# Optimization experiments

Hardware: AMD Instinct MI355X
Metric: run time of the kernel (lower is better)

Reference implementation:

```python
import jax, jax.numpy as jnp
import numpy as np

VAR_N, LEVELS, NCELLS, PRED_N = 4, 17, 56, 12
D = VAR_N * LEVELS          # 68
FLAT = VAR_N * D            # 272 = ntiles * interm in CrossConnector
T = 4096
DT = 0.1                    # fused-ODE solver step of the LTC cell


def _var_encoder(x, w1, b1, w2, b2, w3, b3, w4, b4, w5, b5):
    # nn.Sequential(Linear, ReLU, Linear, ReLU, Linear, ReLU, Linear, ReLU, Linear)
    h = jax.nn.relu(x @ w1 + b1)
    h = jax.nn.relu(h @ w2 + b2)
    h = jax.nn.relu(h @ w3 + b3)
    h = jax.nn.relu(h @ w4 + b4)
    return h @ w5 + b5


def _run_ltc(seq, wx, wh, b, a, tau, wout, bout):
    def cell(h, u):
        f = jax.nn.sigmoid(u @ wx + h @ wh + b)           # gated synaptic activation
        return (h + DT * f * a) / (1.0 + DT * (1.0 / (tau + 0.5) + f))

    def step_obs(h, u):
        h2 = cell(h, u)
        return h2, h2 @ wout + bout

    hT, vs1 = jax.lax.scan(step_obs, jnp.zeros((NCELLS,), seq.dtype), seq)

    def step_pred(carry, _):
        h, v = carry
        h2 = cell(h, v)
        v2 = h2 @ wout + bout
        return (h2, v2), v2

    _, vs2 = jax.lax.scan(step_pred, (hT, vs1[-1]), None, length=PRED_N)
    return jnp.concatenate([vs1, vs2], axis=0)        # (T+PRED_N, LEVELS)


def setup_inputs() -> dict:
    key = jax.random.key(0)
    ks = iter(jax.random.split(key, 64))
    d = {"x": jax.random.normal(next(ks), (T, D), jnp.float32)}

    def add_ve(prefix, inp, out):
        dims = [(inp, inp), (inp, inp), (inp, out), (out, out), (out, out)]
        for i, (fi, fo) in enumerate(dims, 1):
            d[f"{prefix}w{i}"] = jax.random.normal(next(ks), (fi, fo), jnp.float32) / np.sqrt(fi)
            d[f"{prefix}b{i}"] = jax.random.normal(next(ks), (fo,), jnp.float32) * 0.01

    add_ve("p", D, D)          # preproc  VarEncoder(68,68)
    add_ve("c1", LEVELS, D)    # CrossConnector inner VarEncoder(17,68)
    add_ve("c2", FLAT, D)      # CrossConnector outer VarEncoder(272,68)

    d["ltc_wx"] = jax.random.normal(next(ks), (VAR_N, LEVELS, NCELLS), jnp.float32) / np.sqrt(LEVELS)
    d["ltc_wh"] = jax.random.normal(next(ks), (VAR_N, NCELLS, NCELLS), jnp.float32) / np.sqrt(NCELLS)
    d["ltc_b"] = jax.random.normal(next(ks), (VAR_N, NCELLS), jnp.float32) * 0.01
    d["ltc_a"] = jax.random.normal(next(ks), (VAR_N, NCELLS), jnp.float32)
    d["ltc_tau"] = jax.random.uniform(next(ks), (VAR_N, NCELLS), jnp.float32)
    d["ltc_wout"] = jax.random.normal(next(ks), (VAR_N, NCELLS, LEVELS), jnp.float32) / np.sqrt(NCELLS)
    d["ltc_bout"] = jax.random.normal(next(ks), (VAR_N, LEVELS), jnp.float32) * 0.01
    return d


def reference(x, pw1, pb1, pw2, pb2, pw3, pb3, pw4, pb4, pw5, pb5,
              c1w1, c1b1, c1w2, c1b2, c1w3, c1b3, c1w4, c1b4, c1w5, c1b5,
              c2w1, c2b1, c2w2, c2b2, c2w3, c2b3, c2w4, c2b4, c2w5, c2b5,
              ltc_wx, ltc_wh, ltc_b, ltc_a, ltc_tau, ltc_wout, ltc_bout):
    pre = _var_encoder(x, pw1, pb1, pw2, pb2, pw3, pb3, pw4, pb4, pw5, pb5)   # (T, 68)
    xs = pre.reshape(VAR_N, -1, LEVELS)                                       # (4, T, 17) row-major, as torch.reshape
    vs = jax.vmap(_run_ltc)(xs, ltc_wx, ltc_wh, ltc_b, ltc_a, ltc_tau,
                            ltc_wout, ltc_bout)                               # (4, T+12, 17)
    vs = jnp.transpose(vs, (1, 0, 2))                                         # (T+12, 4, 17)
    y = jax.nn.relu(_var_encoder(vs, c1w1, c1b1, c1w2, c1b2, c1w3, c1b3,
                                 c1w4, c1b4, c1w5, c1b5))                     # (T+12, 4, 68)
    y = y.reshape(y.shape[0], -1)                                             # (T+12, 272)
    return _var_encoder(y, c2w1, c2b1, c2w2, c2b2, c2w3, c2b3,
                        c2w4, c2b4, c2w5, c2b5)                               # (T+12, 68)
```

## Files before the change

### kernel.cpp

```cpp
#include <hip/hip_runtime.h>
#include <hip/hip_bf16.h>
#include <math.h>

#define VAR_N 4
#define LEVELS 17
#define NCELLS 56
#define PRED_N 12
#define TSTEPS 4096
#define DT 0.1f
#define RPB 8
#define LOG2E 1.44269504088896340736f

static __device__ __forceinline__ float rl(float x, int lane) {
    return __int_as_float(__builtin_amdgcn_readlane(__float_as_int(x), lane));
}
static __device__ __forceinline__ float rcpf(float x) {
    return __builtin_amdgcn_rcpf(x);
}

template <int S>
__global__ void mlp5_kernel(const float* __restrict__ in, float* __restrict__ out,
                            const float* __restrict__ w1, const float* __restrict__ b1,
                            const float* __restrict__ w2, const float* __restrict__ b2,
                            const float* __restrict__ w3, const float* __restrict__ b3,
                            const float* __restrict__ w4, const float* __restrict__ b4,
                            const float* __restrict__ w5, const float* __restrict__ b5,
                            int nrows, int d0, int d1, int d2, int d3, int d4, int d5,
                            int relu_last) {
    extern __shared__ float lds[];
    float* bufA = lds;
    float* bufB = lds + RPB * S;
    const int r0 = blockIdx.x * RPB;
    const int tid = threadIdx.x;
    const int bt = blockDim.x;

    for (int idx = tid; idx < RPB * d0; idx += bt) {
        int r = idx / d0, c = idx - r * d0;
        int gr = r0 + r;
        bufA[r * S + c] = (gr < nrows) ? in[(size_t)gr * d0 + c] : 0.f;
    }
    __syncthreads();

    const float* Ws[5] = {w1, w2, w3, w4, w5};
    const float* Bs[5] = {b1, b2, b3, b4, b5};
    int dins[5] = {d0, d1, d2, d3, d4};
    int douts[5] = {d1, d2, d3, d4, d5};

    for (int L = 0; L < 5; ++L) {
        const float* __restrict__ W = Ws[L];
        const float* __restrict__ B = Bs[L];
        const int din = dins[L], dout = douts[L];
        const bool act = (L < 4) || (relu_last != 0);
        for (int j = tid; j < dout; j += bt) {
            float acc[RPB];
            float bj = B[j];
#pragma unroll
            for (int r = 0; r < RPB; ++r) acc[r] = bj;
            int k = 0;
            for (; k + 4 <= din; k += 4) {
                float w0v = W[(size_t)(k + 0) * dout + j];
                float w1v = W[(size_t)(k + 1) * dout + j];
                float w2v = W[(size_t)(k + 2) * dout + j];
                float w3v = W[(size_t)(k + 3) * dout + j];
#pragma unroll
                for (int r = 0; r < RPB; ++r) {
                    const float4 hx = *(const float4*)(bufA + r * S + k);
                    acc[r] = fmaf(hx.x, w0v,
                              fmaf(hx.y, w1v,
                               fmaf(hx.z, w2v,
                                fmaf(hx.w, w3v, acc[r]))));
                }
            }
            for (; k < din; ++k) {
                float wv = W[(size_t)k * dout + j];
#pragma unroll
                for (int r = 0; r < RPB; ++r)
                    acc[r] = fmaf(bufA[r * S + k], wv, acc[r]);
            }
#pragma unroll
            for (int r = 0; r < RPB; ++r) {
                float vo = acc[r];
                if (act) vo = fmaxf(vo, 0.f);
                bufB[r * S + j] = vo;
            }
        }
        __syncthreads();
        float* t = bufA; bufA = bufB; bufB = t;
    }

    for (int idx = tid; idx < RPB * d5; idx += bt) {
        int r = idx / d5, c = idx - r * d5;
        int gr = r0 + r;
        if (gr < nrows) out[(size_t)gr * d5 + c] = bufA[r * S + c];
    }
}

__global__ void gprep_kernel(const float* __restrict__ pre, const float* __restrict__ wx,
                             const float* __restrict__ b, float* __restrict__ g) {
    int idx = blockIdx.x * blockDim.x + threadIdx.x;
    if (idx >= VAR_N * NCELLS * TSTEPS) return;
    int t = idx % TSTEPS;
    int rem = idx / TSTEPS;
    int j = rem % NCELLS;
    int v = rem / NCELLS;
    const float* u = pre + (size_t)(v * 1024 + (t >> 2)) * 68 + (t & 3) * LEVELS;
    float acc = b[v * NCELLS + j];
#pragma unroll
    for (int l = 0; l < LEVELS; ++l)
        acc = fmaf(u[l], wx[(v * LEVELS + l) * NCELLS + j], acc);
    g[idx] = acc * LOG2E;
}

__global__ void __launch_bounds__(64, 1) scan_kernel(
    const float* __restrict__ g, const float* __restrict__ wh,
    const float* __restrict__ a, const float* __restrict__ tau,
    const float* __restrict__ wx, const float* __restrict__ wout,
    const float* __restrict__ bout, const float* __restrict__ b,
    float* __restrict__ H, float* __restrict__ vs_t) {
    typedef float v2 __attribute__((ext_vector_type(2)));
    const int v = blockIdx.x;
    const int lane = threadIdx.x;
    const bool active = lane < NCELLS;
    const int j = active ? lane : (NCELLS - 1);
    __shared__ __align__(16) float hbuf[64];

    v2 whp[28];
#pragma unroll
    for (int q = 0; q < 28; ++q) {
        float w0 = active ? wh[((size_t)v * NCELLS + 2 * q + 0) * NCELLS + lane] * LOG2E : 0.f;
        float w1 = active ? wh[((size_t)v * NCELLS + 2 * q + 1) * NCELLS + lane] * LOG2E : 0.f;
        v2 t; t.x = w0; t.y = w1;
        whp[q] = t;
    }
    const float alpha = active ? DT * a[v * NCELLS + lane] : 0.f;
    const float cden = active ? 1.f + DT / (tau[v * NCELLS + lane] + 0.5f) : 1.f;

    const float4* __restrict__ gv4 = (const float4*)(g + ((size_t)v * NCELLS + j) * TSTEPS);
    float* __restrict__ hp = H + (size_t)v * TSTEPS * NCELLS + lane;

    auto cell = [&](float h, float gcur) -> float {
        hbuf[lane] = h;
        const float4* h4 = (const float4*)hbuf;
        float4 hv[14];
#pragma unroll
        for (int q = 0; q < 14; ++q) hv[q] = h4[q];
        v2 a0 = {0.f, 0.f}, a1 = {0.f, 0.f}, a2 = {0.f, 0.f}, a3 = {0.f, 0.f};
#pragma unroll
        for (int q = 0; q < 7; ++q) {
            float4 hq0 = hv[2 * q];
            float4 hq1 = hv[2 * q + 1];
            v2 p0; p0.x = hq0.x; p0.y = hq0.y;
            v2 p1; p1.x = hq0.z; p1.y = hq0.w;
            v2 p2; p2.x = hq1.x; p2.y = hq1.y;
            v2 p3; p3.x = hq1.z; p3.y = hq1.w;
            a0 = __builtin_elementwise_fma(p0, whp[4 * q + 0], a0);
            a1 = __builtin_elementwise_fma(p1, whp[4 * q + 1], a1);
            a2 = __builtin_elementwise_fma(p2, whp[4 * q + 2], a2);
            a3 = __builtin_elementwise_fma(p3, whp[4 * q + 3], a3);
        }
        v2 s = (a0 + a1) + (a2 + a3);
        float z2 = (gcur + s.x) + s.y;
        float zc = fmaxf(z2, -80.f);
        float e = __builtin_amdgcn_exp2f(-zc);
        float t1 = 1.f + e;
        float num = fmaf(h, t1, alpha);
        float den = fmaf(cden, t1, DT);
        float hn = num * rcpf(den);
        __builtin_amdgcn_sched_group_barrier(0x200, 1, 0);
        __builtin_amdgcn_sched_group_barrier(0x100, 14, 0);
        __builtin_amdgcn_sched_group_barrier(0x002, 40, 0);
        return hn;
    };

    float h = 0.f;
    float4 gq = gv4[0];
    for (int tq = 0; tq < TSTEPS / 4; ++tq) {
        float4 gn = gq;
        if (tq + 1 < TSTEPS / 4) gn = gv4[tq + 1];
        h = cell(h, gq.x); if (active) hp[0 * NCELLS] = h;
        h = cell(h, gq.y); if (active) hp[1 * NCELLS] = h;
        h = cell(h, gq.z); if (active) hp[2 * NCELLS] = h;
        h = cell(h, gq.w); if (active) hp[3 * NCELLS] = h;
        hp += 4 * NCELLS;
        gq = gn;
    }

    float wxcol[LEVELS];
#pragma unroll
    for (int l = 0; l < LEVELS; ++l)
        wxcol[l] = active ? wx[(v * LEVELS + l) * NCELLS + lane] * LOG2E : 0.f;
    float wtc[NCELLS];
#pragma unroll
    for (int jj = 0; jj < NCELLS; ++jj)
        wtc[jj] = (lane < LEVELS) ? wout[((size_t)v * NCELLS + jj) * LEVELS + lane] : 0.f;
    const float bj = active ? b[v * NCELLS + lane] * LOG2E : 0.f;
    const float boutl = (lane < LEVELS) ? bout[v * LEVELS + lane] : 0.f;

    float vv = boutl;
#pragma unroll
    for (int jj = 0; jj < NCELLS; ++jj) vv = fmaf(rl(h, jj), wtc[jj], vv);

    for (int i = 0; i < PRED_N; ++i) {
        float z2 = bj;
#pragma unroll
        for (int l = 0; l < LEVELS; ++l) z2 = fmaf(rl(vv, l), wxcol[l], z2);
#pragma unroll
        for (int k = 0; k < NCELLS; ++k) {
            float wk = (k & 1) ? whp[k >> 1].y : whp[k >> 1].x;
            z2 = fmaf(rl(h, k), wk, z2);
        }
        float zc = fmaxf(z2, -80.f);
        float e = __builtin_amdgcn_exp2f(-zc);
        float t1 = 1.f + e;
        h = fmaf(h, t1, alpha) * rcpf(fmaf(cden, t1, DT));
        vv = boutl;
#pragma unroll
        for (int jj = 0; jj < NCELLS; ++jj) vv = fmaf(rl(h, jj), wtc[jj], vv);
        if (lane < LEVELS)
            vs_t[((size_t)(TSTEPS + i) * VAR_N + v) * LEVELS + lane] = vv;
    }
}

__global__ void proj_kernel(const float* __restrict__ H, const float* __restrict__ wout,
                            const float* __restrict__ bout, float* __restrict__ vs_t) {
    int idx = blockIdx.x * blockDim.x + threadIdx.x;
    if (idx >= VAR_N * TSTEPS * LEVELS) return;
    int l = idx % LEVELS;
    int rem = idx / LEVELS;
    int t = rem % TSTEPS;
    int v = rem / TSTEPS;
    const float* hrow = H + ((size_t)v * TSTEPS + t) * NCELLS;
    float acc = bout[v * LEVELS + l];
#pragma unroll
    for (int jj = 0; jj < NCELLS; ++jj)
        acc = fmaf(hrow[jj], wout[(v * NCELLS + jj) * LEVELS + l], acc);
    vs_t[((size_t)t * VAR_N + v) * LEVELS + l] = acc;
}

extern "C" void kernel_launch(void* const* d_in, const int* in_sizes, int n_in,
                              void* d_out, int out_size, void* d_ws, size_t ws_size,
                              hipStream_t stream) {
    const float* x = (const float*)d_in[0];
    const float* pw[5] = {(const float*)d_in[1], (const float*)d_in[3], (const float*)d_in[5],
                          (const float*)d_in[7], (const float*)d_in[9]};
    const float* pb[5] = {(const float*)d_in[2], (const float*)d_in[4], (const float*)d_in[6],
                          (const float*)d_in[8], (const float*)d_in[10]};
    const float* c1w[5] = {(const float*)d_in[11], (const float*)d_in[13], (const float*)d_in[15],
                           (const float*)d_in[17], (const float*)d_in[19]};
    const float* c1b[5] = {(const float*)d_in[12], (const float*)d_in[14], (const float*)d_in[16],
                           (const float*)d_in[18], (const float*)d_in[20]};
    const float* c2w[5] = {(const float*)d_in[21], (const float*)d_in[23], (const float*)d_in[25],
                           (const float*)d_in[27], (const float*)d_in[29]};
    const float* c2b[5] = {(const float*)d_in[22], (const float*)d_in[24], (const float*)d_in[26],
                           (const float*)d_in[28], (const float*)d_in[30]};
    const float* ltc_wx = (const float*)d_in[31];
    const float* ltc_wh = (const float*)d_in[32];
    const float* ltc_b = (const float*)d_in[33];
    const float* ltc_a = (const float*)d_in[34];
    const float* ltc_tau = (const float*)d_in[35];
    const float* ltc_wout = (const float*)d_in[36];
    const float* ltc_bout = (const float*)d_in[37];

    float* ws = (float*)d_ws;
    float* pre = ws;
    float* g = pre + 278528;
    float* H = g + 917504;
    float* vs_t = H + 917504;
    float* y1 = vs_t + 279344;
    float* out = (float*)d_out;

    const int TROWS = TSTEPS + PRED_N;

    {
        int nrows = TSTEPS;
        int blocks = (nrows + RPB - 1) / RPB;
        size_t shmem = 2 * RPB * 68 * sizeof(float);
        mlp5_kernel<68><<<blocks, 256, shmem, stream>>>(
            x, pre, pw[0], pb[0], pw[1], pb[1], pw[2], pb[2], pw[3], pb[3], pw[4], pb[4],
            nrows, 68, 68, 68, 68, 68, 68, 0);
    }
    {
        int n = VAR_N * NCELLS * TSTEPS;
        gprep_kernel<<<(n + 255) / 256, 256, 0, stream>>>(pre, ltc_wx, ltc_b, g);
    }
    scan_kernel<<<VAR_N, 64, 0, stream>>>(g, ltc_wh, ltc_a, ltc_tau, ltc_wx,
                                          ltc_wout, ltc_bout, ltc_b, H, vs_t);
    {
        int n = VAR_N * TSTEPS * LEVELS;
        proj_kernel<<<(n + 255) / 256, 256, 0, stream>>>(H, ltc_wout, ltc_bout, vs_t);
    }
    {
        int nrows = TROWS * VAR_N;
        int blocks = (nrows + RPB - 1) / RPB;
        size_t shmem = 2 * RPB * 68 * sizeof(float);
        mlp5_kernel<68><<<blocks, 256, shmem, stream>>>(
            vs_t, y1, c1w[0], c1b[0], c1w[1], c1b[1], c1w[2], c1b[2], c1w[3], c1b[3],
            c1w[4], c1b[4], nrows, 17, 17, 17, 68, 68, 68, 1);
    }
    {
        int nrows = TROWS;
        int blocks = (nrows + RPB - 1) / RPB;
        size_t shmem = 2 * RPB * 272 * sizeof(float);
        mlp5_kernel<272><<<blocks, 256, shmem, stream>>>(
            y1, out, c2w[0], c2b[0], c2w[1], c2b[1], c2w[2], c2b[2], c2w[3], c2b[3],
            c2w[4], c2b[4], nrows, 272, 272, 272, 68, 68, 68, 0);
    }
}
```

Baseline: 1.078 ms.

## Fuse preproc with gate prep, fold projection into scan, fuse cross-connector MLPs

Merges the preproc MLP and the input-gate precompute into one kernel, computes the output projection inside the recurrent scan from the pre-update hidden state, and fuses the two cross-connector MLPs into one kernel with the intermediate kept in shared memory. This removes the H buffer, the proj kernel and the y1/pre round trips along with three launches. In exchange, the serial scan does extra packed FMAs per step, which may lengthen its critical path.

```diff
diff --git a/kernel.cpp b/kernel.cpp
--- a/kernel.cpp
+++ b/kernel.cpp
@@ -7,6 +7,7 @@
 #define NCELLS 56
 #define PRED_N 12
 #define TSTEPS 4096
+#define TROWS (TSTEPS + PRED_N)
 #define DT 0.1f
 #define RPB 8
 #define LOG2E 1.44269504088896340736f
@@ -18,97 +19,70 @@
     return __builtin_amdgcn_rcpf(x);
 }
 
-template <int S>
-__global__ void mlp5_kernel(const float* __restrict__ in, float* __restrict__ out,
-                            const float* __restrict__ w1, const float* __restrict__ b1,
-                            const float* __restrict__ w2, const float* __restrict__ b2,
-                            const float* __restrict__ w3, const float* __restrict__ b3,
-                            const float* __restrict__ w4, const float* __restrict__ b4,
-                            const float* __restrict__ w5, const float* __restrict__ b5,
-                            int nrows, int d0, int d1, int d2, int d3, int d4, int d5,
-                            int relu_last) {
-    extern __shared__ float lds[];
+__global__ void pre_g_kernel(const float* __restrict__ x,
+                             const float* __restrict__ w1, const float* __restrict__ b1,
+                             const float* __restrict__ w2, const float* __restrict__ b2,
+                             const float* __restrict__ w3, const float* __restrict__ b3,
+                             const float* __restrict__ w4, const float* __restrict__ b4,
+                             const float* __restrict__ w5, const float* __restrict__ b5,
+                             const float* __restrict__ wx, const float* __restrict__ bvec,
+                             float* __restrict__ g) {
+    __shared__ float lds[2 * RPB * 68];
     float* bufA = lds;
-    float* bufB = lds + RPB * S;
+    float* bufB = lds + RPB * 68;
     const int r0 = blockIdx.x * RPB;
     const int tid = threadIdx.x;
-    const int bt = blockDim.x;
-
-    for (int idx = tid; idx < RPB * d0; idx += bt) {
-        int r = idx / d0, c = idx - r * d0;
-        int gr = r0 + r;
-        bufA[r * S + c] = (gr < nrows) ? in[(size_t)gr * d0 + c] : 0.f;
-    }
+
+    for (int idx = tid; idx < RPB * 68; idx += 256)
+        bufA[idx] = x[(size_t)r0 * 68 + idx];
     __syncthreads();
 
     const float* Ws[5] = {w1, w2, w3, w4, w5};
     const float* Bs[5] = {b1, b2, b3, b4, b5};
-    int dins[5] = {d0, d1, d2, d3, d4};
-    int douts[5] = {d1, d2, d3, d4, d5};
-
     for (int L = 0; L < 5; ++L) {
         const float* __restrict__ W = Ws[L];
-        const float* __restrict__ B = Bs[L];
-        const int din = dins[L], dout = douts[L];
-        const bool act = (L < 4) || (relu_last != 0);
-        for (int j = tid; j < dout; j += bt) {
+        const bool act = (L < 4);
+        if (tid < 68) {
+            const int j = tid;
             float acc[RPB];
-            float bj = B[j];
+            float bj = Bs[L][j];
 #pragma unroll
             for (int r = 0; r < RPB; ++r) acc[r] = bj;
-            int k = 0;
-            for (; k + 4 <= din; k += 4) {
-                float w0v = W[(size_t)(k + 0) * dout + j];
-                float w1v = W[(size_t)(k + 1) * dout + j];
-                float w2v = W[(size_t)(k + 2) * dout + j];
-                float w3v = W[(size_t)(k + 3) * dout + j];
+            for (int k = 0; k + 4 <= 68; k += 4) {
+                float w0v = W[(k + 0) * 68 + j];
+                float w1v = W[(k + 1) * 68 + j];
+                float w2v = W[(k + 2) * 68 + j];
+                float w3v = W[(k + 3) * 68 + j];
 #pragma unroll
                 for (int r = 0; r < RPB; ++r) {
-                    const float4 hx = *(const float4*)(bufA + r * S + k);
-                    acc[r] = fmaf(hx.x, w0v,
-                              fmaf(hx.y, w1v,
-                               fmaf(hx.z, w2v,
-                                fmaf(hx.w, w3v, acc[r]))));
+                    const float4 hx = *(const float4*)(bufA + r * 68 + k);
+                    acc[r] = fmaf(hx.x, w0v, fmaf(hx.y, w1v,
+                              fmaf(hx.z, w2v, fmaf(hx.w, w3v, acc[r]))));
                 }
             }
-            for (; k < din; ++k) {
-                float wv = W[(size_t)k * dout + j];
-#pragma unroll
-                for (int r = 0; r < RPB; ++r)
-                    acc[r] = fmaf(bufA[r * S + k], wv, acc[r]);
-            }
-#pragma unroll
-            for (int r = 0; r < RPB; ++r) {
-                float vo = acc[r];
-                if (act) vo = fmaxf(vo, 0.f);
-                bufB[r * S + j] = vo;
-            }
+#pragma unroll
+            for (int r = 0; r < RPB; ++r)
+                bufB[r * 68 + j] = act ? fmaxf(acc[r], 0.f) : acc[r];
         }
         __syncthreads();
         float* t = bufA; bufA = bufB; bufB = t;
     }
 
-    for (int idx = tid; idx < RPB * d5; idx += bt) {
-        int r = idx / d5, c = idx - r * d5;
+    for (int idx = tid; idx < RPB * 4 * NCELLS; idx += 256) {
+        int r = idx / 224;
+        int rem = idx - r * 224;
+        int q = rem / NCELLS;
+        int j = rem - q * NCELLS;
         int gr = r0 + r;
-        if (gr < nrows) out[(size_t)gr * d5 + c] = bufA[r * S + c];
-    }
-}
-
-__global__ void gprep_kernel(const float* __restrict__ pre, const float* __restrict__ wx,
-                             const float* __restrict__ b, float* __restrict__ g) {
-    int idx = blockIdx.x * blockDim.x + threadIdx.x;
-    if (idx >= VAR_N * NCELLS * TSTEPS) return;
-    int t = idx % TSTEPS;
-    int rem = idx / TSTEPS;
-    int j = rem % NCELLS;
-    int v = rem / NCELLS;
-    const float* u = pre + (size_t)(v * 1024 + (t >> 2)) * 68 + (t & 3) * LEVELS;
-    float acc = b[v * NCELLS + j];
-#pragma unroll
-    for (int l = 0; l < LEVELS; ++l)
-        acc = fmaf(u[l], wx[(v * LEVELS + l) * NCELLS + j], acc);
-    g[idx] = acc * LOG2E;
+        int v = gr >> 10;
+        int trow = ((gr & 1023) << 2) + q;
+        const float* arow = bufA + r * 68 + q * LEVELS;
+        float acc = bvec[v * NCELLS + j];
+#pragma unroll
+        for (int l = 0; l < LEVELS; ++l)
+            acc = fmaf(arow[l], wx[(v * LEVELS + l) * NCELLS + j], acc);
+        g[((size_t)(v * NCELLS + j)) * TSTEPS + trow] = acc * LOG2E;
+    }
 }
 
 __global__ void __launch_bounds__(64, 1) scan_kernel(
@@ -116,7 +90,7 @@
     const float* __restrict__ a, const float* __restrict__ tau,
     const float* __restrict__ wx, const float* __restrict__ wout,
     const float* __restrict__ bout, const float* __restrict__ b,
-    float* __restrict__ H, float* __restrict__ vs_t) {
+    float* __restrict__ vs_t) {
     typedef float v2 __attribute__((ext_vector_type(2)));
     const int v = blockIdx.x;
     const int lane = threadIdx.x;
@@ -132,19 +106,29 @@
         v2 t; t.x = w0; t.y = w1;
         whp[q] = t;
     }
+    v2 wtcp[28];
+#pragma unroll
+    for (int q = 0; q < 28; ++q) {
+        float w0 = (lane < LEVELS) ? wout[((size_t)v * NCELLS + 2 * q + 0) * LEVELS + lane] : 0.f;
+        float w1 = (lane < LEVELS) ? wout[((size_t)v * NCELLS + 2 * q + 1) * LEVELS + lane] : 0.f;
+        v2 t; t.x = w0; t.y = w1;
+        wtcp[q] = t;
+    }
     const float alpha = active ? DT * a[v * NCELLS + lane] : 0.f;
     const float cden = active ? 1.f + DT / (tau[v * NCELLS + lane] + 0.5f) : 1.f;
+    const float boutl = (lane < LEVELS) ? bout[v * LEVELS + lane] : 0.f;
 
     const float4* __restrict__ gv4 = (const float4*)(g + ((size_t)v * NCELLS + j) * TSTEPS);
-    float* __restrict__ hp = H + (size_t)v * TSTEPS * NCELLS + lane;
-
-    auto cell = [&](float h, float gcur) -> float {
+    float* __restrict__ vsb = vs_t + (size_t)v * LEVELS + lane;
+
+    auto cell = [&](float h, float gcur, float& vsv) -> float {
         hbuf[lane] = h;
         const float4* h4 = (const float4*)hbuf;
         float4 hv[14];
 #pragma unroll
         for (int q = 0; q < 14; ++q) hv[q] = h4[q];
         v2 a0 = {0.f, 0.f}, a1 = {0.f, 0.f}, a2 = {0.f, 0.f}, a3 = {0.f, 0.f};
+        v2 u0 = {0.f, 0.f}, u1 = {0.f, 0.f}, u2 = {0.f, 0.f}, u3 = {0.f, 0.f};
 #pragma unroll
         for (int q = 0; q < 7; ++q) {
             float4 hq0 = hv[2 * q];
@@ -157,8 +141,14 @@
             a1 = __builtin_elementwise_fma(p1, whp[4 * q + 1], a1);
             a2 = __builtin_elementwise_fma(p2, whp[4 * q + 2], a2);
             a3 = __builtin_elementwise_fma(p3, whp[4 * q + 3], a3);
+            u0 = __builtin_elementwise_fma(p0, wtcp[4 * q + 0], u0);
+            u1 = __builtin_elementwise_fma(p1, wtcp[4 * q + 1], u1);
+            u2 = __builtin_elementwise_fma(p2, wtcp[4 * q + 2], u2);
+            u3 = __builtin_elementwise_fma(p3, wtcp[4 * q + 3], u3);
         }
         v2 s = (a0 + a1) + (a2 + a3);
+        v2 us = (u0 + u1) + (u2 + u3);
+        vsv = (boutl + us.x) + us.y;
         float z2 = (gcur + s.x) + s.y;
         float zc = fmaxf(z2, -80.f);
         float e = __builtin_amdgcn_exp2f(-zc);
@@ -168,20 +158,26 @@
         float hn = num * rcpf(den);
         __builtin_amdgcn_sched_group_barrier(0x200, 1, 0);
         __builtin_amdgcn_sched_group_barrier(0x100, 14, 0);
-        __builtin_amdgcn_sched_group_barrier(0x002, 40, 0);
+        __builtin_amdgcn_sched_group_barrier(0x002, 72, 0);
         return hn;
     };
 
+    const bool vlane = lane < LEVELS;
     float h = 0.f;
+    float vsv;
     float4 gq = gv4[0];
     for (int tq = 0; tq < TSTEPS / 4; ++tq) {
         float4 gn = gq;
         if (tq + 1 < TSTEPS / 4) gn = gv4[tq + 1];
-        h = cell(h, gq.x); if (active) hp[0 * NCELLS] = h;
-        h = cell(h, gq.y); if (active) hp[1 * NCELLS] = h;
-        h = cell(h, gq.z); if (active) hp[2 * NCELLS] = h;
-        h = cell(h, gq.w); if (active) hp[3 * NCELLS] = h;
-        hp += 4 * NCELLS;
+        const size_t tb = (size_t)(4 * tq) * VAR_N * LEVELS;
+        h = cell(h, gq.x, vsv);
+        if (tq > 0 && vlane) vsb[tb - (size_t)VAR_N * LEVELS] = vsv;
+        h = cell(h, gq.y, vsv);
+        if (vlane) vsb[tb] = vsv;
+        h = cell(h, gq.z, vsv);
+        if (vlane) vsb[tb + (size_t)VAR_N * LEVELS] = vsv;
+        h = cell(h, gq.w, vsv);
+        if (vlane) vsb[tb + (size_t)2 * VAR_N * LEVELS] = vsv;
         gq = gn;
     }
 
@@ -189,16 +185,15 @@
 #pragma unroll
     for (int l = 0; l < LEVELS; ++l)
         wxcol[l] = active ? wx[(v * LEVELS + l) * NCELLS + lane] * LOG2E : 0.f;
-    float wtc[NCELLS];
-#pragma unroll
-    for (int jj = 0; jj < NCELLS; ++jj)
-        wtc[jj] = (lane < LEVELS) ? wout[((size_t)v * NCELLS + jj) * LEVELS + lane] : 0.f;
     const float bj = active ? b[v * NCELLS + lane] * LOG2E : 0.f;
-    const float boutl = (lane < LEVELS) ? bout[v * LEVELS + lane] : 0.f;
 
     float vv = boutl;
 #pragma unroll
-    for (int jj = 0; jj < NCELLS; ++jj) vv = fmaf(rl(h, jj), wtc[jj], vv);
+    for (int k = 0; k < NCELLS; ++k) {
+        float wk = (k & 1) ? wtcp[k >> 1].y : wtcp[k >> 1].x;
+        vv = fmaf(rl(h, k), wk, vv);
+    }
+    if (vlane) vsb[(size_t)(TSTEPS - 1) * VAR_N * LEVELS] = vv;
 
     for (int i = 0; i < PRED_N; ++i) {
         float z2 = bj;
@@ -215,26 +210,127 @@
         h = fmaf(h, t1, alpha) * rcpf(fmaf(cden, t1, DT));
         vv = boutl;
 #pragma unroll
-        for (int jj = 0; jj < NCELLS; ++jj) vv = fmaf(rl(h, jj), wtc[jj], vv);
-        if (lane < LEVELS)
-            vs_t[((size_t)(TSTEPS + i) * VAR_N + v) * LEVELS + lane] = vv;
-    }
-}
-
-__global__ void proj_kernel(const float* __restrict__ H, const float* __restrict__ wout,
-                            const float* __restrict__ bout, float* __restrict__ vs_t) {
-    int idx = blockIdx.x * blockDim.x + threadIdx.x;
-    if (idx >= VAR_N * TSTEPS * LEVELS) return;
-    int l = idx % LEVELS;
-    int rem = idx / LEVELS;
-    int t = rem % TSTEPS;
-    int v = rem / TSTEPS;
-    const float* hrow = H + ((size_t)v * TSTEPS + t) * NCELLS;
-    float acc = bout[v * LEVELS + l];
-#pragma unroll
-    for (int jj = 0; jj < NCELLS; ++jj)
-        acc = fmaf(hrow[jj], wout[(v * NCELLS + jj) * LEVELS + l], acc);
-    vs_t[((size_t)t * VAR_N + v) * LEVELS + l] = acc;
+        for (int k = 0; k < NCELLS; ++k) {
+            float wk = (k & 1) ? wtcp[k >> 1].y : wtcp[k >> 1].x;
+            vv = fmaf(rl(h, k), wk, vv);
+        }
+        if (vlane) vsb[(size_t)(TSTEPS + i) * VAR_N * LEVELS] = vv;
+    }
+}
+
+#define TB 8
+
+static __device__ __forceinline__ void layer32(const float* __restrict__ in, int si,
+                                               float* __restrict__ outb, int so,
+                                               const float* __restrict__ W,
+                                               const float* __restrict__ B,
+                                               int din, int dout, bool act, int tid) {
+    if (tid < dout) {
+        const int j = tid;
+        float acc[32];
+        float bj = B[j];
+#pragma unroll
+        for (int r = 0; r < 32; ++r) acc[r] = bj;
+        int k = 0;
+        for (; k + 4 <= din; k += 4) {
+            float w0 = W[(k + 0) * dout + j];
+            float w1 = W[(k + 1) * dout + j];
+            float w2 = W[(k + 2) * dout + j];
+            float w3 = W[(k + 3) * dout + j];
+#pragma unroll
+            for (int r = 0; r < 32; ++r) {
+                const float4 hx = *(const float4*)(in + r * si + k);
+                acc[r] = fmaf(hx.x, w0, fmaf(hx.y, w1,
+                          fmaf(hx.z, w2, fmaf(hx.w, w3, acc[r]))));
+            }
+        }
+        for (; k < din; ++k) {
+            float wv = W[k * dout + j];
+#pragma unroll
+            for (int r = 0; r < 32; ++r) acc[r] = fmaf(in[r * si + k], wv, acc[r]);
+        }
+#pragma unroll
+        for (int r = 0; r < 32; ++r)
+            outb[r * so + j] = act ? fmaxf(acc[r], 0.f) : acc[r];
+    }
+}
+
+static __device__ __forceinline__ void layer8(const float* __restrict__ in,
+                                              float* __restrict__ outb,
+                                              const float* __restrict__ W,
+                                              const float* __restrict__ B,
+                                              int din, int dout, bool act, int tid) {
+    for (int j = tid; j < dout; j += 256) {
+        float acc[TB];
+        float bj = B[j];
+#pragma unroll
+        for (int r = 0; r < TB; ++r) acc[r] = bj;
+        int k = 0;
+        for (; k + 4 <= din; k += 4) {
+            float w0 = W[(size_t)(k + 0) * dout + j];
+            float w1 = W[(size_t)(k + 1) * dout + j];
+            float w2 = W[(size_t)(k + 2) * dout + j];
+            float w3 = W[(size_t)(k + 3) * dout + j];
+#pragma unroll
+            for (int r = 0; r < TB; ++r) {
+                const float4 hx = *(const float4*)(in + r * 272 + k);
+                acc[r] = fmaf(hx.x, w0, fmaf(hx.y, w1,
+                          fmaf(hx.z, w2, fmaf(hx.w, w3, acc[r]))));
+            }
+        }
+        for (; k < din; ++k) {
+            float wv = W[(size_t)k * dout + j];
+#pragma unroll
+            for (int r = 0; r < TB; ++r) acc[r] = fmaf(in[r * 272 + k], wv, acc[r]);
+        }
+#pragma unroll
+        for (int r = 0; r < TB; ++r)
+            outb[r * 272 + j] = act ? fmaxf(acc[r], 0.f) : acc[r];
+    }
+}
+
+__global__ void c1c2_kernel(const float* __restrict__ vs,
+                            const float* __restrict__ c1w1, const float* __restrict__ c1b1,
+                            const float* __restrict__ c1w2, const float* __restrict__ c1b2,
+                            const float* __restrict__ c1w3, const float* __restrict__ c1b3,
+                            const float* __restrict__ c1w4, const float* __restrict__ c1b4,
+                            const float* __restrict__ c1w5, const float* __restrict__ c1b5,
+                            const float* __restrict__ c2w1, const float* __restrict__ c2b1,
+                            const float* __restrict__ c2w2, const float* __restrict__ c2b2,
+                            const float* __restrict__ c2w3, const float* __restrict__ c2b3,
+                            const float* __restrict__ c2w4, const float* __restrict__ c2b4,
+                            const float* __restrict__ c2w5, const float* __restrict__ c2b5,
+                            float* __restrict__ out) {
+    __shared__ __align__(16) float bA[32 * 20];
+    __shared__ __align__(16) float bB[32 * 20];
+    __shared__ __align__(16) float bY[TB * 272];
+    __shared__ __align__(16) float bZ[TB * 272];
+    const int t0 = blockIdx.x * TB;
+    const int tid = threadIdx.x;
+
+    for (int idx = tid; idx < TB * 4 * LEVELS; idx += 256) {
+        int row = idx / LEVELS, l = idx - row * LEVELS;
+        int t = t0 + (row >> 2);
+        bA[row * 20 + l] = (t < TROWS) ? vs[((size_t)t * VAR_N + (row & 3)) * LEVELS + l] : 0.f;
+    }
+    __syncthreads();
+
+    layer32(bA, 20, bB, 20, c1w1, c1b1, 17, 17, true, tid);  __syncthreads();
+    layer32(bB, 20, bA, 20, c1w2, c1b2, 17, 17, true, tid);  __syncthreads();
+    layer32(bA, 20, bY, 68, c1w3, c1b3, 17, 68, true, tid);  __syncthreads();
+    layer32(bY, 68, bZ, 68, c1w4, c1b4, 68, 68, true, tid);  __syncthreads();
+    layer32(bZ, 68, bY, 68, c1w5, c1b5, 68, 68, true, tid);  __syncthreads();
+    layer8(bY, bZ, c2w1, c2b1, 272, 272, true, tid);  __syncthreads();
+    layer8(bZ, bY, c2w2, c2b2, 272, 272, true, tid);  __syncthreads();
+    layer8(bY, bZ, c2w3, c2b3, 272, 68, true, tid);   __syncthreads();
+    layer8(bZ, bY, c2w4, c2b4, 68, 68, true, tid);    __syncthreads();
+    layer8(bY, bZ, c2w5, c2b5, 68, 68, false, tid);   __syncthreads();
+
+    for (int idx = tid; idx < TB * 68; idx += 256) {
+        int tq = idx / 68, c = idx - tq * 68;
+        int t = t0 + tq;
+        if (t < TROWS) out[(size_t)t * 68 + c] = bZ[tq * 272 + c];
+    }
 }
 
 extern "C" void kernel_launch(void* const* d_in, const int* in_sizes, int n_in,
@@ -262,47 +358,20 @@
     const float* ltc_bout = (const float*)d_in[37];
 
     float* ws = (float*)d_ws;
-    float* pre = ws;
-    float* g = pre + 278528;
-    float* H = g + 917504;
-    float* vs_t = H + 917504;
-    float* y1 = vs_t + 279344;
+    float* g = ws;
+    float* vs_t = g + 917504;
     float* out = (float*)d_out;
 
-    const int TROWS = TSTEPS + PRED_N;
-
-    {
-        int nrows = TSTEPS;
-        int blocks = (nrows + RPB - 1) / RPB;
-        size_t shmem = 2 * RPB * 68 * sizeof(float);
-        mlp5_kernel<68><<<blocks, 256, shmem, stream>>>(
-            x, pre, pw[0], pb[0], pw[1], pb[1], pw[2], pb[2], pw[3], pb[3], pw[4], pb[4],
-            nrows, 68, 68, 68, 68, 68, 68, 0);
-    }
-    {
-        int n = VAR_N * NCELLS * TSTEPS;
-        gprep_kernel<<<(n + 255) / 256, 256, 0, stream>>>(pre, ltc_wx, ltc_b, g);
-    }
+    pre_g_kernel<<<TSTEPS / RPB, 256, 0, stream>>>(
+        x, pw[0], pb[0], pw[1], pb[1], pw[2], pb[2], pw[3], pb[3], pw[4], pb[4],
+        ltc_wx, ltc_b, g);
+
     scan_kernel<<<VAR_N, 64, 0, stream>>>(g, ltc_wh, ltc_a, ltc_tau, ltc_wx,
-                                          ltc_wout, ltc_bout, ltc_b, H, vs_t);
-    {
-        int n = VAR_N * TSTEPS * LEVELS;
-        proj_kernel<<<(n + 255) / 256, 256, 0, stream>>>(H, ltc_wout, ltc_bout, vs_t);
-    }
-    {
-        int nrows = TROWS * VAR_N;
-        int blocks = (nrows + RPB - 1) / RPB;
-        size_t shmem = 2 * RPB * 68 * sizeof(float);
-        mlp5_kernel<68><<<blocks, 256, shmem, stream>>>(
-            vs_t, y1, c1w[0], c1b[0], c1w[1], c1b[1], c1w[2], c1b[2], c1w[3], c1b[3],
-            c1w[4], c1b[4], nrows, 17, 17, 17, 68, 68, 68, 1);
-    }
-    {
-        int nrows = TROWS;
-        int blocks = (nrows + RPB - 1) / RPB;
-        size_t shmem = 2 * RPB * 272 * sizeof(float);
-        mlp5_kernel<272><<<blocks, 256, shmem, stream>>>(
-            y1, out, c2w[0], c2b[0], c2w[1], c2b[1], c2w[2], c2b[2], c2w[3], c2b[3],
-            c2w[4], c2b[4], nrows, 272, 272, 272, 68, 68, 68, 0);
-    }
-}
+                                          ltc_wout, ltc_bout, ltc_b, vs_t);
+
+    c1c2_kernel<<<(TROWS + TB - 1) / TB, 256, 0, stream>>>(
+        vs_t,
+        c1w[0], c1b[0], c1w[1], c1b[1], c1w[2], c1b[2], c1w[3], c1b[3], c1w[4], c1b[4],
+        c2w[0], c2b[0], c2w[1], c2b[1], c2w[2], c2b[2], c2w[3], c2b[3], c2w[4], c2b[4],
+        out);
+}
```

After: 1.334 ms. 1.24x slower.
